# Kernel tuning notes

Measured on AMD Instinct MI355X. Metric: run time of the kernel, lower is better.

The kernel has to match this reference:

```python
import jax, jax.numpy as jnp
import numpy as np

EPS = 1e-30


def _logmmexp(P, logW):
    """Stable logsumexp_k(P[..., k] + logW[a, k]) -> (..., a) via max-shifted matmul."""
    mP = jnp.max(P, axis=-1, keepdims=True)          # (..., 1)
    mW = jnp.max(logW, axis=-1, keepdims=True)       # (A, 1)
    out = jnp.einsum('...k,ak->...a', jnp.exp(P - mP), jnp.exp(logW - mW))
    return jnp.log(out) + mP + mW[:, 0]


def _inside_chart(tokens, log_binary, log_lexical):
    B, L = tokens.shape
    N = log_binary.shape[0]
    chart = jnp.full((B, N, L, L + 1), -jnp.inf, dtype=log_lexical.dtype)
    # Base case: chart[:, :, i, i+1] = log_lexical[:, tokens[:, i]]
    lex = jnp.transpose(log_lexical[:, tokens], (1, 0, 2))  # (B, N, L)
    ii = jnp.arange(L)
    chart = chart.at[:, :, ii, ii + 1].set(lex)
    # CKY recursion: loop over span length (structural, static), vectorize over
    # start positions i and split points k.
    for s in range(2, L + 1):
        pos = L - s + 1
        i = np.arange(pos)
        m = np.arange(s - 1)
        k_idx = i[:, None] + m[None, :] + 1                 # (pos, s-1) split points
        left = chart[:, :, i[:, None], k_idx]               # (B, N, pos, s-1)
        right = chart[:, :, k_idx, (i + s)[:, None]]        # (B, N, pos, s-1)
        lt = jnp.transpose(left, (0, 2, 3, 1))              # (B, pos, m, N_B)
        rt = jnp.transpose(right, (0, 2, 3, 1))             # (B, pos, m, N_C)
        # P[b,i,m,B,C] = left + right
        P = lt[..., :, None] + rt[..., None, :]             # (B, pos, m, N, N)
        Pf = P.reshape(B, pos, (s - 1) * N * N)
        logW = jnp.broadcast_to(log_binary[:, None, :, :], (N, s - 1, N, N)).reshape(N, -1)
        scores = _logmmexp(Pf, logW)                        # (B, pos, N_A)
        chart = chart.at[:, :, i, i + s].set(jnp.transpose(scores, (0, 2, 1)))
    return chart


def setup_inputs() -> dict:
    key = jax.random.key(0)
    k1, k2, k3 = jax.random.split(key, 3)
    B, L, N, T = 32, 32, 48, 32000
    tokens = jax.random.randint(k1, (B, L), 0, T)
    binary = jax.random.uniform(k2, (N, N, N), dtype=jnp.float32)
    lexical = jax.random.uniform(k3, (N, T), dtype=jnp.float32)
    return {"tokens": tokens, "binary": binary, "lexical": lexical}


def reference(tokens, binary, lexical):
    start = 0
    log_binary = jnp.log(jnp.clip(binary, EPS))
    log_lexical = jnp.log(jnp.clip(lexical, EPS))
    chart = _inside_chart(tokens, log_binary, log_lexical)
    return chart[:, start, 0, tokens.shape[1]]  # (B,) sentence log-probs
```

## Files before the change

### kernel.cpp

```cpp
#include <hip/hip_runtime.h>
#include <math.h>

#define NNT 48
#define LL 32
#define BB 32
#define N2 2304
#define KSTEPS 72
#define EPSV 1e-30f
#define CH_J ((LL+1)*NNT)
#define SEB_S 2328
#define PD_RS 20
#define PD_T  328
#define PD_W  984
#define NCELL (BB*LL*(LL+1)*NNT)

typedef __attribute__((ext_vector_type(8))) short bf16x8;
typedef __attribute__((ext_vector_type(4))) float f32x4;
typedef __attribute__((ext_vector_type(4))) int   i32x4;

__device__ __forceinline__ int ch_idx(int b, int i, int j, int n) {
    return (((b*LL + i)*(LL+1) + j)*NNT + n);
}
__device__ __forceinline__ unsigned short f2bf(float x) {
    unsigned u = __float_as_uint(x);
    u = (u + 0x7fffu + ((u >> 16) & 1u)) >> 16;
    return (unsigned short)u;
}
__device__ __forceinline__ int cvtpk(float lo, float hi) {
    int r;
    asm("v_cvt_pk_bf16_f32 %0, %1, %2" : "=v"(r) : "v"(lo), "v"(hi));
    return r;
}
__device__ __forceinline__ int uvt_base(int q, int r, int kc) {
    return q*1536 + ((((r << 2) + kc) ^ (r & 7)) << 3);
}
__device__ __forceinline__ float wavemax(float x) {
    #pragma unroll
    for (int o = 32; o; o >>= 1) x = fmaxf(x, __shfl_xor(x, o));
    return x;
}
__device__ __forceinline__ float ch_ld(const float* p) {
    return __hip_atomic_load(p, __ATOMIC_RELAXED, __HIP_MEMORY_SCOPE_AGENT);
}
__device__ __forceinline__ void ch_st(float* p, float v) {
    __hip_atomic_store(p, v, __ATOMIC_RELAXED, __HIP_MEMORY_SCOPE_AGENT);
}
#define LBAR() { asm volatile("s_waitcnt lgkmcnt(0)" ::: "memory"); \
                 __builtin_amdgcn_s_barrier(); }

__global__ void prep_kernel(const float* __restrict__ binary, const int* __restrict__ tokens,
                            const float* __restrict__ lexical, unsigned short* __restrict__ Wp,
                            float* __restrict__ chart, int T) {
    if (blockIdx.x < 432) {
        int idx = blockIdx.x*256 + threadIdx.x;
        int j  = idx & 7;
        int l  = (idx >> 3) & 63;
        int ks = (idx >> 9) % KSTEPS;
        int nt = idx / (KSTEPS*512);
        int e = ks*32 + ((l >> 4) << 3) + j;
        int n = nt*16 + (l & 15);
        int bp = e % 48, c = e / 48;
        Wp[idx] = f2bf(fmaxf(binary[n*N2 + bp*48 + c], EPSV));
    } else if (blockIdx.x < 688) {
        int row = (blockIdx.x - 432)*4 + (threadIdx.x >> 6);
        int lane = threadIdx.x & 63;
        int b = row >> 5, i = row & 31;
        int tok = tokens[b*LL + i];
        float val = (lane < NNT)
            ? __logf(fmaxf(lexical[(size_t)lane*(size_t)T + (size_t)tok], EPSV))
            : -INFINITY;
        float rm = wavemax(val);
        if (lane < NNT) chart[ch_idx(b, i, i+1, lane)] = val;
        if (lane == 0) chart[ch_idx(b, i, 0, i+1)] = rm;
    } else {
        int idx = (blockIdx.x - 688)*256 + threadIdx.x;
        if (idx < NCELL) {
            int n = idx % NNT;
            int r = idx / NNT;
            int j = r % (LL + 1);
            int i = (r / (LL + 1)) % LL;
            if (j != i + 1 && !(j == 0 && n == i + 1))
                chart[idx] = -INFINITY;
        }
    }
}

#define MFMA16(A,B,C) __builtin_amdgcn_mfma_f32_16x16x32_bf16(A,B,C,0,0,0)

#define LDV(V, C)                                                              \
    { _Pragma("unroll")                                                        \
      for (int dt = 0; dt < 8; ++dt) {                                         \
          int t = (C)*8 + dt; int tt = (t < tc) ? t : tc - 1;                  \
          int kk = rr + tt*2;                                                  \
          V[dt] = ch_ld(vp + kk*CH_J + ln);                                    \
      } }
#define FRESHFIX(V)                                                            \
    { if (freshLDS) {                                                          \
          if (lane == 0) bt = sRm[q + 1][s - 1];                               \
          if (rr == 0) V[0] = sOut[q + 1][ln];                                 \
      } }
#define CONSCH(V, C)                                                           \
    { int pv[4];                                                               \
      _Pragma("unroll")                                                        \
      for (int dp = 0; dp < 4; ++dp) {                                         \
          int t0 = (C)*8 + 2*dp;                                               \
          int tt0 = (t0     < tc) ? t0     : tc - 1;                           \
          int tt1 = (t0 + 1 < tc) ? t0 + 1 : tc - 1;                           \
          float a0 = sRm[q][rr + tt0*2 + 1];                                   \
          float a1 = sRm[q][rr + tt1*2 + 1];                                   \
          float e0 = __expf(V[2*dp]     + a0 - M);                             \
          float e1 = __expf(V[2*dp + 1] + a1 - M);                             \
          pv[dp] = cvtpk(e0, e1);                                              \
      }                                                                        \
      if (lane < NNT) {                                                        \
          int ad = uvt_base(w, lane, (C));                                     \
          *(i32x4*)&sUV[12288 + ad] = (i32x4){pv[0],pv[1],pv[2],pv[3]};        \
      } }

__global__ __launch_bounds__(512, 2) void inside_kernel(
        const unsigned short* __restrict__ Wp,
        float* __restrict__ chart,
        float* __restrict__ out) {
    const int pb = blockIdx.x;
    const int b = pb & 31, c = pb >> 5;
    const int i_base = 28 - 4*c;
    const int tid = threadIdx.x, lane = tid & 63, w = tid >> 6;
    const int fr = lane & 15, kg = lane >> 4;
    const int ln = (lane < NNT) ? lane : 0;
    const int q = w >> 1, rr = w & 1;
    const int i0 = i_base + q;

    __shared__ __align__(16) short sUV[24576];
    __shared__ __align__(16) short sEb[16*SEB_S];
    __shared__ float pD[8*PD_W];
    __shared__ float sRm[4][33];
    __shared__ float sOut[4][NNT];

    for (int x = tid; x < 12288; x += 512) ((int*)sUV)[x] = 0;
    for (int x = tid; x < 18624; x += 512) ((int*)sEb)[x] = 0;
    if (tid < 4)
        sRm[tid][1] = ch_ld(&chart[ch_idx(b, i_base + tid, 0, i_base + tid + 1)]);
    if (w < 4 && lane < NNT)
        sOut[w][lane] = ch_ld(&chart[ch_idx(b, i_base + w, i_base + w + 1, lane)]);

    const bf16x8* wp8 = (const bf16x8*)Wp;
    const int kstart = 9*w;
    bf16x8 wreg[9][3];
    #pragma unroll
    for (int t = 0; t < 9; ++t)
        #pragma unroll
        for (int nt = 0; nt < 3; ++nt)
            wreg[t][nt] = wp8[(nt*KSTEPS + kstart + t)*64 + lane];

    __syncthreads();

    for (int s = 2; s <= LL; ++s) {
        const int nk = s - 1;
        if (i_base > LL - s) return;

        const bool active = (i0 <= LL - s);
        const int tc = active ? ((nk - rr + 1) >> 1) : 0;
        const bool freshLDS = active && (s > 2) && (q < 3);
        float M = -INFINITY;
        f32x4 ea[9];
        #pragma unroll
        for (int z = 0; z < 9; ++z) ea[z] = (f32x4){0.f, 0.f, 0.f, 0.f};

        if (active && rr == ((nk - 1) & 1) && lane < NNT) {
            int tn = (nk - 1 - rr) >> 1;
            float eu = __expf(sOut[q][lane] - sRm[q][s - 1]);
            sUV[uvt_base(w, lane, tn >> 3) + (tn & 7)] = (short)f2bf(eu);
        }

        if (tc > 0) {
            const float* vp = chart + ch_idx(b, i0 + 1, i0 + s, 0);
            const float* bp = chart + ch_idx(b, i0 + 1, 0, i0 + s);

            float vv0[8], vv1[8];
            float bt = (lane < nk) ? ch_ld(bp + lane*CH_J) : 0.f;
            LDV(vv0, 0)
            if (tc > 8) { LDV(vv1, 1) }
            FRESHFIX(vv0)
            for (;;) {
                bool bad = (lane < nk) && (bt == -INFINITY);
                #pragma unroll
                for (int dt = 0; dt < 8; ++dt) bad |= (vv0[dt] == -INFINITY);
                if (tc > 8) {
                    #pragma unroll
                    for (int dt = 0; dt < 8; ++dt) bad |= (vv1[dt] == -INFINITY);
                }
                if (!__any(bad)) break;
                bt = (lane < nk) ? ch_ld(bp + lane*CH_J) : 0.f;
                LDV(vv0, 0)
                if (tc > 8) { LDV(vv1, 1) }
                FRESHFIX(vv0)
            }

            {
                float al = (lane < nk) ? sRm[q][lane + 1] : -INFINITY;
                M = wavemax((lane < nk) ? al + bt : -INFINITY);
            }

            CONSCH(vv0, 0)
            if (tc > 8) { CONSCH(vv1, 1) }

            bf16x8 A0 = *(const bf16x8*)&sUV[uvt_base(w,  0 + fr, kg)];
            bf16x8 A1 = *(const bf16x8*)&sUV[uvt_base(w, 16 + fr, kg)];
            bf16x8 A2 = *(const bf16x8*)&sUV[uvt_base(w, 32 + fr, kg)];
            bf16x8 B0 = *(const bf16x8*)&sUV[12288 + uvt_base(w,  0 + fr, kg)];
            bf16x8 B1 = *(const bf16x8*)&sUV[12288 + uvt_base(w, 16 + fr, kg)];
            bf16x8 B2 = *(const bf16x8*)&sUV[12288 + uvt_base(w, 32 + fr, kg)];
            ea[0] = MFMA16(A0,B0,ea[0]); ea[1] = MFMA16(A0,B1,ea[1]); ea[2] = MFMA16(A0,B2,ea[2]);
            ea[3] = MFMA16(A1,B0,ea[3]); ea[4] = MFMA16(A1,B1,ea[4]); ea[5] = MFMA16(A1,B2,ea[5]);
            ea[6] = MFMA16(A2,B0,ea[6]); ea[7] = MFMA16(A2,B1,ea[7]); ea[8] = MFMA16(A2,B2,ea[8]);
        }

        if (active) {
            #pragma unroll
            for (int mt = 0; mt < 3; ++mt) {
                #pragma unroll
                for (int ct = 0; ct < 3; ++ct) {
                    f32x4 d = ea[mt*3 + ct];
                    int e0 = (ct*16 + fr)*48 + mt*16 + kg*4;
                    unsigned lo = (unsigned)cvtpk(d[0], d[1]);
                    unsigned hi = (unsigned)cvtpk(d[2], d[3]);
                    *(unsigned long long*)&sEb[w*SEB_S + e0] =
                        (unsigned long long)lo | ((unsigned long long)hi << 32);
                }
            }
        }

        LBAR();

        {
            f32x4 c0 = {0.f,0.f,0.f,0.f}, c1 = c0, c2 = c0;
            #pragma unroll
            for (int t = 0; t < 9; ++t) {
                bf16x8 af = *(const bf16x8*)&sEb[fr*SEB_S + (kstart + t)*32 + kg*8];
                c0 = MFMA16(af, wreg[t][0], c0);
                c1 = MFMA16(af, wreg[t][1], c1);
                c2 = MFMA16(af, wreg[t][2], c2);
            }
            #pragma unroll
            for (int r2 = 0; r2 < 4; ++r2) {
                int row = kg*4 + r2;
                pD[w*PD_W + 0*PD_T + row*PD_RS + fr] = c0[r2];
                pD[w*PD_W + 1*PD_T + row*PD_RS + fr] = c1[r2];
                pD[w*PD_W + 2*PD_T + row*PD_RS + fr] = c2[r2];
            }
        }
        LBAR();

        if (active && rr == 0) {
            float sum = 0.f;
            #pragma unroll
            for (int w2 = 0; w2 < 8; ++w2) {
                const float* pp = &pD[w2*PD_W + (ln >> 4)*PD_T + (ln & 15)];
                sum += pp[(2*q)*PD_RS] + pp[(2*q + 1)*PD_RS];
            }
            float val = M + __logf(sum);
            float rm = wavemax((lane < NNT) ? val : -INFINITY);
            if (lane < NNT) {
                ch_st(&chart[ch_idx(b, i0, i0 + s, lane)], val);
                sOut[q][lane] = val;
            }
            if (lane == 0) {
                ch_st(&chart[ch_idx(b, i0, 0, i0 + s)], rm);
                sRm[q][s] = rm;
                if (s == LL) out[b] = val;
            }
        }
        LBAR();
    }
}

extern "C" void kernel_launch(void* const* d_in, const int* in_sizes, int n_in,
                              void* d_out, int out_size, void* d_ws, size_t ws_size,
                              hipStream_t stream) {
    const int*   tokens  = (const int*)d_in[0];
    const float* binary  = (const float*)d_in[1];
    const float* lexical = (const float*)d_in[2];
    float* out = (float*)d_out;

    float* chart = (float*)d_ws;
    unsigned short* Wp = (unsigned short*)(chart + (size_t)NCELL);

    int T = in_sizes[2] / NNT;

    int fill_blocks = (NCELL + 255)/256;
    prep_kernel<<<688 + fill_blocks, 256, 0, stream>>>(binary, tokens, lexical, Wp, chart, T);
    inside_kernel<<<256, 512, 0, stream>>>(Wp, chart, out);
}
```

Before: 119.7 us.

## Prefetch next span's chart operands during current step

Loads the right-child values and row maxima for the next span length into registers at the end of the current iteration, before the barrier, instead of at the start of the next iteration. The global-memory load latency is meant to overlap with the epilogue and barrier wait. The existing retry loop that spins while it sees -inf values handles stale prefetched data. The cost is more register pressure and possible extra retry loads when the prefetch reads cells that are not yet written.

```diff
diff --git a/kernel.cpp b/kernel.cpp
--- a/kernel.cpp
+++ b/kernel.cpp
@@ -87,16 +87,16 @@
 
 #define MFMA16(A,B,C) __builtin_amdgcn_mfma_f32_16x16x32_bf16(A,B,C,0,0,0)
 
-#define LDV(V, C)                                                              \
+#define LDVP(V, C, TCX, VPX)                                                   \
     { _Pragma("unroll")                                                        \
       for (int dt = 0; dt < 8; ++dt) {                                         \
-          int t = (C)*8 + dt; int tt = (t < tc) ? t : tc - 1;                  \
+          int t = (C)*8 + dt; int tt = (t < (TCX)) ? t : (TCX) - 1;            \
           int kk = rr + tt*2;                                                  \
-          V[dt] = ch_ld(vp + kk*CH_J + ln);                                    \
+          V[dt] = ch_ld((VPX) + kk*CH_J + ln);                                 \
       } }
 #define FRESHFIX(V)                                                            \
     { if (freshLDS) {                                                          \
-          if (lane == 0) bt = sRm[q + 1][s - 1];                               \
+          if (lane == 0) btP = sRm[q + 1][s - 1];                              \
           if (rr == 0) V[0] = sOut[q + 1][ln];                                 \
       } }
 #define CONSCH(V, C)                                                           \
@@ -152,6 +152,17 @@
         for (int nt = 0; nt < 3; ++nt)
             wreg[t][nt] = wp8[(nt*KSTEPS + kstart + t)*64 + lane];
 
+    float vvP0[8] = {0,0,0,0,0,0,0,0}, vvP1[8] = {0,0,0,0,0,0,0,0}, btP = 0.f;
+    if (i0 <= LL - 2) {
+        const int nkn = 1, tcn = (nkn - rr + 1) >> 1;
+        if (tcn > 0) {
+            const float* vpn = chart + ch_idx(b, i0 + 1, i0 + 2, 0);
+            const float* bpn = chart + ch_idx(b, i0 + 1, 0, i0 + 2);
+            btP = (lane < nkn) ? ch_ld(bpn + lane*CH_J) : 0.f;
+            LDVP(vvP0, 0, tcn, vpn)
+        }
+    }
+
     __syncthreads();
 
     for (int s = 2; s <= LL; ++s) {
@@ -176,33 +187,29 @@
             const float* vp = chart + ch_idx(b, i0 + 1, i0 + s, 0);
             const float* bp = chart + ch_idx(b, i0 + 1, 0, i0 + s);
 
-            float vv0[8], vv1[8];
-            float bt = (lane < nk) ? ch_ld(bp + lane*CH_J) : 0.f;
-            LDV(vv0, 0)
-            if (tc > 8) { LDV(vv1, 1) }
-            FRESHFIX(vv0)
+            FRESHFIX(vvP0)
             for (;;) {
-                bool bad = (lane < nk) && (bt == -INFINITY);
+                bool bad = (lane < nk) && (btP == -INFINITY);
                 #pragma unroll
-                for (int dt = 0; dt < 8; ++dt) bad |= (vv0[dt] == -INFINITY);
+                for (int dt = 0; dt < 8; ++dt) bad |= (vvP0[dt] == -INFINITY);
                 if (tc > 8) {
                     #pragma unroll
-                    for (int dt = 0; dt < 8; ++dt) bad |= (vv1[dt] == -INFINITY);
+                    for (int dt = 0; dt < 8; ++dt) bad |= (vvP1[dt] == -INFINITY);
                 }
                 if (!__any(bad)) break;
-                bt = (lane < nk) ? ch_ld(bp + lane*CH_J) : 0.f;
-                LDV(vv0, 0)
-                if (tc > 8) { LDV(vv1, 1) }
-                FRESHFIX(vv0)
+                btP = (lane < nk) ? ch_ld(bp + lane*CH_J) : 0.f;
+                LDVP(vvP0, 0, tc, vp)
+                if (tc > 8) { LDVP(vvP1, 1, tc, vp) }
+                FRESHFIX(vvP0)
             }
 
             {
                 float al = (lane < nk) ? sRm[q][lane + 1] : -INFINITY;
-                M = wavemax((lane < nk) ? al + bt : -INFINITY);
-            }
-
-            CONSCH(vv0, 0)
-            if (tc > 8) { CONSCH(vv1, 1) }
+                M = wavemax((lane < nk) ? al + btP : -INFINITY);
+            }
+
+            CONSCH(vvP0, 0)
+            if (tc > 8) { CONSCH(vvP1, 1) }
 
             bf16x8 A0 = *(const bf16x8*)&sUV[uvt_base(w,  0 + fr, kg)];
             bf16x8 A1 = *(const bf16x8*)&sUV[uvt_base(w, 16 + fr, kg)];
@@ -213,6 +220,16 @@
             ea[0] = MFMA16(A0,B0,ea[0]); ea[1] = MFMA16(A0,B1,ea[1]); ea[2] = MFMA16(A0,B2,ea[2]);
             ea[3] = MFMA16(A1,B0,ea[3]); ea[4] = MFMA16(A1,B1,ea[4]); ea[5] = MFMA16(A1,B2,ea[5]);
             ea[6] = MFMA16(A2,B0,ea[6]); ea[7] = MFMA16(A2,B1,ea[7]); ea[8] = MFMA16(A2,B2,ea[8]);
+        }
+
+        if (s < LL && i0 <= LL - s - 1) {
+            const int nkn = s;
+            const int tcn = (nkn - rr + 1) >> 1;
+            const float* vpn = chart + ch_idx(b, i0 + 1, i0 + s + 1, 0);
+            const float* bpn = chart + ch_idx(b, i0 + 1, 0, i0 + s + 1);
+            btP = (lane < nkn) ? ch_ld(bpn + lane*CH_J) : 0.f;
+            LDVP(vvP0, 0, tcn, vpn)
+            if (tcn > 8) { LDVP(vvP1, 1, tcn, vpn) }
         }
 
         if (active) {
```

After: 127.3 us. 6.4% more time.
